# Kernel optimization log

Measured on AMD Instinct MI355X. Metric: run time of the kernel, lower is better.

## Reference

```python
import jax, jax.numpy as jnp
import numpy as np

EMBED_DIM = 768
NUM_HEADS = 12
HEAD_DIM = EMBED_DIM // NUM_HEADS


def setup_inputs() -> dict:
    key = jax.random.key(0)
    ks = jax.random.split(key, 6)
    B, N = 8, 1024
    x = jax.random.normal(ks[0], (B, N, EMBED_DIM), dtype=jnp.float32)
    pos_embedding = jax.random.normal(ks[1], (1, NUM_HEADS, N, N), dtype=jnp.float32)
    s_in = 1.0 / np.sqrt(EMBED_DIM)
    W_qkv = jax.random.normal(ks[2], (EMBED_DIM, 3 * EMBED_DIM), dtype=jnp.float32) * s_in
    b_qkv = jnp.zeros((3 * EMBED_DIM,), dtype=jnp.float32)
    W_proj = jax.random.normal(ks[3], (EMBED_DIM, EMBED_DIM), dtype=jnp.float32) * s_in
    b_proj = jnp.zeros((EMBED_DIM,), dtype=jnp.float32)
    return {"x": x, "pos_embedding": pos_embedding, "W_qkv": W_qkv,
            "b_qkv": b_qkv, "W_proj": W_proj, "b_proj": b_proj}


def reference(x, pos_embedding, W_qkv, b_qkv, W_proj, b_proj):
    B, N, C = x.shape
    H, D = NUM_HEADS, HEAD_DIM
    qkv = x @ W_qkv + b_qkv                      # [B,N,3C]
    qkv = qkv.reshape(B, N, 3, H, D)
    q = qkv[:, :, 0].transpose(0, 2, 1, 3)       # [B,H,N,D]
    k = qkv[:, :, 1].transpose(0, 2, 1, 3)
    v = qkv[:, :, 2].transpose(0, 2, 1, 3)
    # NOTE: bias is added BEFORE scaling, matching the original module.
    scores = (jnp.einsum('bhnd,bhmd->bhnm', q, k) + pos_embedding) / jnp.sqrt(
        jnp.asarray(D, dtype=x.dtype))
    attn = jax.nn.softmax(scores, axis=-1)       # dropout is identity in eval
    out = jnp.einsum('bhnm,bhmd->bhnd', attn, v)
    out = out.transpose(0, 2, 1, 3).reshape(B, N, C)
    return out @ W_proj + b_proj
```

## Files before the change

kernel.cpp:

```cpp
#include <hip/hip_runtime.h>

#define SEQ   1024
#define HEADS 12
#define CDIM  768
#define BATCH 8

#define QSCALE 0.18033688011112042f

typedef __attribute__((ext_vector_type(8))) short bf16x8;
typedef __attribute__((ext_vector_type(4))) float f32x4;
typedef __attribute__((ext_vector_type(16))) float f32x16;
typedef __attribute__((ext_vector_type(4))) float float4v;
typedef __attribute__((ext_vector_type(4))) short short4v;

__device__ __forceinline__ void gload_lds16(const void* g, void* l) {
  __builtin_amdgcn_global_load_lds(
      (const __attribute__((address_space(1))) unsigned int*)g,
      (__attribute__((address_space(3))) unsigned int*)l, 16, 0, 0);
}

__device__ __forceinline__ unsigned short f2bf(float f) {
  union { float f; unsigned u; } v; v.f = f;
  unsigned r = v.u + 0x7fff + ((v.u >> 16) & 1);
  return (unsigned short)(r >> 16);
}

__device__ __forceinline__ unsigned cvtpk(float a, float b) {
  unsigned r;
  asm("v_cvt_pk_bf16_f32 %0, %1, %2" : "=v"(r) : "v"(a), "v"(b));
  return r;
}

__device__ __forceinline__ float bfsel(unsigned u, int odd) {
  union { unsigned u; float f; } v;
  v.u = odd ? (u & 0xffff0000u) : (u << 16);
  return v.f;
}

__global__ __launch_bounds__(256) void prep_x_kernel(const float* __restrict__ x,
                                                     short* __restrict__ A) {
  int i = blockIdx.x * 256 + threadIdx.x;
  int r = i / 192;
  int c4 = (i % 192) * 4;
  float4v xv = *(const float4v*)(x + (size_t)r * 768 + c4);
  short4v hi;
#pragma unroll
  for (int j = 0; j < 4; ++j) hi[j] = (short)f2bf(xv[j]);
  *(short4v*)(A + (size_t)r * 768 + c4) = hi;
}

__global__ __launch_bounds__(256) void prep_w_kernel(const float* __restrict__ W,
                                                     short* __restrict__ Bt) {
  __shared__ float tile[64][65];
  int k0 = blockIdx.x * 64;
  int n0 = blockIdx.y * 64;
  int t = threadIdx.x;
#pragma unroll
  for (int it = 0; it < 16; ++it) {
    int r = it * 4 + (t >> 6);
    int c = t & 63;
    tile[r][c] = W[(size_t)(k0 + r) * 2304 + n0 + c];
  }
  __syncthreads();
#pragma unroll
  for (int it = 0; it < 16; ++it) {
    int nr = it * 4 + (t >> 6);
    int kc = t & 63;
    Bt[(size_t)(n0 + nr) * 768 + k0 + kc] = (short)f2bf(tile[kc][nr]);
  }
}

__global__ __launch_bounds__(256) void prep_wp_kernel(const float* __restrict__ W,
                                                      short* __restrict__ Bt) {
  __shared__ float tile[64][65];
  int k0 = blockIdx.x * 64;
  int n0 = blockIdx.y * 64;
  int t = threadIdx.x;
#pragma unroll
  for (int it = 0; it < 16; ++it) {
    int r = it * 4 + (t >> 6);
    int c = t & 63;
    tile[r][c] = W[(size_t)(k0 + r) * 768 + n0 + c];
  }
  __syncthreads();
#pragma unroll
  for (int it = 0; it < 16; ++it) {
    int nr = it * 4 + (t >> 6);
    int kc = t & 63;
    Bt[(size_t)(n0 + nr) * 768 + k0 + kc] = (short)f2bf(tile[kc][nr]);
  }
}

__global__ __launch_bounds__(256) void prep_pos_kernel(const float* __restrict__ P,
                                                       short* __restrict__ PB) {
  int t = blockIdx.x * 256 + threadIdx.x;
  int lane = t & 63;
  int jh   = (t >> 6) & 1;
  int i0   = (t >> 7) & 1;
  int w    = (t >> 8) & 3;
  int ti   = (t >> 10) & 15;
  int qblk = (t >> 14) & 7;
  int h    = t >> 17;
  int c5 = lane & 31, g1 = lane >> 5;
  int q = qblk * 128 + w * 32 + c5;
  const float* src = P + ((size_t)h * SEQ + q) * SEQ
                     + ti * 64 + i0 * 32 + 4 * g1 + 16 * jh;
  float4v v0 = *(const float4v*)(src);
  float4v v1 = *(const float4v*)(src + 8);
  union { short s[8]; bf16x8 v; } o;
#pragma unroll
  for (int p = 0; p < 4; ++p) {
    o.s[p]     = (short)f2bf(v0[p] * QSCALE);
    o.s[4 + p] = (short)f2bf(v1[p] * QSCALE);
  }
  *(bf16x8*)(PB + (size_t)t * 8) = o.v;
}

template <int MODE>
__global__ __launch_bounds__(512, 4) void gemm_kernel(
    const short* __restrict__ A, const short* __restrict__ Bt,
    const float* __restrict__ bias,
    short* __restrict__ outQ, short* __restrict__ outK, short* __restrict__ outVT,
    float* __restrict__ outF) {
  constexpr int NBLK = (MODE == 1) ? 18 : 6;
  constexpr int CHUNK = (MODE == 1) ? 144 : 48;
  const int bid = blockIdx.x;
  const int lb = (bid & 7) * CHUNK + (bid >> 3);
  const int n0 = (lb % NBLK) * 128;
  const int m0 = (lb / NBLK) * 128;

  __shared__ short Als[2][128 * 64];
  __shared__ short Bls[2][128 * 64];
  const int tid = threadIdx.x;
  const int lane = tid & 63;
  const int w = tid >> 6;
  const int wr = (w & 1) * 64;
  const int wc = (w >> 1) * 32;
  f32x4 acc[4][2];
#pragma unroll
  for (int mi = 0; mi < 4; ++mi)
#pragma unroll
    for (int ni = 0; ni < 2; ++ni) acc[mi][ni] = (f32x4){0.f, 0.f, 0.f, 0.f};

  auto STAGE = [&](int buf, int k0) {
#pragma unroll
    for (int pass = 0; pass < 2; ++pass) {
      int rbase = pass * 64 + w * 8;
      int row = rbase + (lane >> 3);
      int ul = (lane & 7) ^ (row & 7);
      gload_lds16(A + (size_t)(m0 + row) * 768 + k0 + ul * 8, Als[buf] + rbase * 64);
      gload_lds16(Bt + (size_t)(n0 + row) * 768 + k0 + ul * 8, Bls[buf] + rbase * 64);
    }
  };

  STAGE(0, 0);
  asm volatile("s_waitcnt vmcnt(0)" ::: "memory");
  __builtin_amdgcn_sched_barrier(0);
  __builtin_amdgcn_s_barrier();

  for (int t = 0; t < 12; ++t) {
    if (t < 11) STAGE((t + 1) & 1, (t + 1) * 64);
    const short* Ab = Als[t & 1];
    const short* Bb = Bls[t & 1];
    __builtin_amdgcn_s_setprio(1);
#pragma unroll
    for (int kk = 0; kk < 2; ++kk) {
      bf16x8 af[4], bfv[2];
#pragma unroll
      for (int mi = 0; mi < 4; ++mi) {
        int row = wr + mi * 16 + (lane & 15);
        int off = (row * 128 + kk * 64 + (lane >> 4) * 16) ^ ((row & 7) << 4);
        af[mi] = *(const bf16x8*)((const char*)Ab + off);
      }
#pragma unroll
      for (int ni = 0; ni < 2; ++ni) {
        int row = wc + ni * 16 + (lane & 15);
        int off = (row * 128 + kk * 64 + (lane >> 4) * 16) ^ ((row & 7) << 4);
        bfv[ni] = *(const bf16x8*)((const char*)Bb + off);
      }
#pragma unroll
      for (int mi = 0; mi < 4; ++mi)
#pragma unroll
        for (int ni = 0; ni < 2; ++ni)
          acc[mi][ni] = __builtin_amdgcn_mfma_f32_16x16x32_bf16(
              af[mi], bfv[ni], acc[mi][ni], 0, 0, 0);
    }
    __builtin_amdgcn_s_setprio(0);
    if (t < 11) {
      asm volatile("s_waitcnt vmcnt(0)" ::: "memory");
      __builtin_amdgcn_sched_barrier(0);
      __builtin_amdgcn_s_barrier();
    }
  }

  if (MODE == 1) {
    const int three = n0 / 768;
    const int nb = n0 - three * 768;
#pragma unroll
    for (int mi = 0; mi < 4; ++mi)
#pragma unroll
      for (int ni = 0; ni < 2; ++ni)
#pragma unroll
        for (int j = 0; j < 4; ++j) {
          int row = m0 + wr + mi * 16 + ((lane >> 4) << 2) + j;
          int col = n0 + wc + ni * 16 + (lane & 15);
          float v = acc[mi][ni][j] + bias[col];
          int rem = nb + wc + ni * 16 + (lane & 15);
          int hh = rem >> 6, d = rem & 63;
          int b = row >> 10, n = row & 1023;
          size_t bh = (size_t)(b * 12 + hh);
          if (three == 0)      outQ[(bh * 1024 + n) * 64 + d] = (short)f2bf(v * QSCALE);
          else if (three == 1) outK[(bh * 1024 + n) * 64 + d] = (short)f2bf(v);
          else                 outVT[(bh * 64 + d) * 1024 + n] = (short)f2bf(v);
        }
  } else {
#pragma unroll
    for (int mi = 0; mi < 4; ++mi)
#pragma unroll
      for (int ni = 0; ni < 2; ++ni)
#pragma unroll
        for (int j = 0; j < 4; ++j) {
          int row = m0 + wr + mi * 16 + ((lane >> 4) << 2) + j;
          int col = n0 + wc + ni * 16 + (lane & 15);
          outF[(size_t)row * 768 + col] = acc[mi][ni][j] + bias[col];
        }
  }
}

#define MKFRAG(B, pA, pB, pC, pD)                                    \
  { unsigned x0 = (pA), y0 = (pC), x1 = (pB), y1 = (pD);             \
    asm("v_permlane32_swap_b32 %0, %1" : "+v"(x0), "+v"(y0));        \
    asm("v_permlane32_swap_b32 %0, %1" : "+v"(x1), "+v"(y1));        \
    B.u[0] = x0; B.u[1] = x1; B.u[2] = y0; B.u[3] = y1; }

__global__ __launch_bounds__(256, 3) void attn_kernel(
    const short* __restrict__ qb, const short* __restrict__ kb,
    const short* __restrict__ vtb, const short* __restrict__ posb,
    short* __restrict__ outb) {
  const int bid = blockIdx.x;
  const int lb = (bid & 7) * 96 + (bid >> 3);
  const int qblk = lb & 7;
  const int hb = lb >> 3;
  const int h = hb >> 3, b = hb & 7;

  const int tid = threadIdx.x, lane = tid & 63, w = tid >> 6;
  const int c5 = lane & 31, g1 = lane >> 5;
  const size_t bh = (size_t)(b * 12 + h);
  const short* Q = qb + bh * SEQ * 64;
  const short* K = kb + bh * SEQ * 64;
  const short* VT = vtb + bh * 64 * SEQ;
  const int q0w = qblk * 128 + w * 32;

  const short* pwb = posb + (size_t)h * 1048576 + (size_t)qblk * 131072
                     + w * 2048 + lane * 8;

  __shared__ short kls[3 * 4096];
  __shared__ short vls[3 * 4096];

  bf16x8 qf[4];
#pragma unroll
  for (int kd = 0; kd < 4; ++kd)
    qf[kd] = *(const bf16x8*)(Q + (size_t)(q0w + c5) * 64 + kd * 16 + g1 * 8);

  f32x16 o0, o1;
#pragma unroll
  for (int i = 0; i < 16; ++i) { o0[i] = 0.f; o1[i] = 0.f; }
  float lsum = 0.f;

  auto STAGE = [&](short* kb_, short* vb_, int kv0) {
    int r0 = w * 8 + (lane >> 3);
    int u0 = (lane & 7) ^ (r0 & 7);
    gload_lds16(K + (size_t)(kv0 + r0) * 64 + u0 * 8, kb_ + w * 512);
    gload_lds16(K + (size_t)(kv0 + 32 + r0) * 64 + u0 * 8, kb_ + 2048 + w * 512);
    gload_lds16(VT + (size_t)r0 * SEQ + kv0 + u0 * 8, vb_ + w * 512);
    gload_lds16(VT + (size_t)(32 + r0) * SEQ + kv0 + u0 * 8, vb_ + 2048 + w * 512);
  };

  short* kbuf0 = kls;        short* vbuf0 = vls;
  short* kbuf1 = kls + 4096; short* vbuf1 = vls + 4096;
  short* kbuf2 = kls + 8192; short* vbuf2 = vls + 8192;

  union pb4 { bf16x8 v; unsigned u[4]; };
  pb4 ua0, ua1, ub0, ub1, na0, na1, nb0, nb1;
  ua0.v = *(const bf16x8*)(pwb);
  ua1.v = *(const bf16x8*)(pwb + 512);
  ub0.v = *(const bf16x8*)(pwb + 1024);
  ub1.v = *(const bf16x8*)(pwb + 1536);
  STAGE(kbuf0, vbuf0, 0);
  STAGE(kbuf1, vbuf1, 64);
  asm volatile("s_waitcnt vmcnt(4)" ::: "memory");
  __builtin_amdgcn_sched_barrier(0);
  __builtin_amdgcn_s_barrier();

  for (int ti = 0; ti < 16; ++ti) {
    const int kv0 = ti * 64;

    if (ti < 15) {
      const short* pnx = pwb + (ti + 1) * 8192;
      na0.v = *(const bf16x8*)(pnx);
      na1.v = *(const bf16x8*)(pnx + 512);
      nb0.v = *(const bf16x8*)(pnx + 1024);
      nb1.v = *(const bf16x8*)(pnx + 1536);
    }
    asm volatile("" ::: "memory");
    if (ti < 14) STAGE(kbuf2, vbuf2, kv0 + 128);

    const short* kc = kbuf0;
    const short* vc = vbuf0;

    f32x16 p0, p1;
#pragma unroll
    for (int i = 0; i < 16; ++i) { p0[i] = 0.f; p1[i] = 0.f; }
    __builtin_amdgcn_s_setprio(1);
#pragma unroll
    for (int kd = 0; kd < 4; ++kd) {
      int off0 = (c5 * 128 + kd * 32 + g1 * 16) ^ ((c5 & 7) << 4);
      int off1 = ((32 + c5) * 128 + kd * 32 + g1 * 16) ^ ((c5 & 7) << 4);
      bf16x8 kf0 = *(const bf16x8*)((const char*)kc + off0);
      bf16x8 kf1 = *(const bf16x8*)((const char*)kc + off1);
      p0 = __builtin_amdgcn_mfma_f32_32x32x16_bf16(kf0, qf[kd], p0, 0, 0, 0);
      p1 = __builtin_amdgcn_mfma_f32_32x32x16_bf16(kf1, qf[kd], p1, 0, 0, 0);
    }
    __builtin_amdgcn_s_setprio(0);

#pragma unroll
    for (int r = 0; r < 16; ++r) {
      unsigned wa = (r < 8) ? ua0.u[(r >> 1) & 3] : ua1.u[(r >> 1) & 3];
      unsigned wb = (r < 8) ? ub0.u[(r >> 1) & 3] : ub1.u[(r >> 1) & 3];
      float a = exp2f(p0[r] + bfsel(wa, r & 1));
      float bq = exp2f(p1[r] + bfsel(wb, r & 1));
      p0[r] = a; p1[r] = bq;
      lsum += a + bq;
    }

    unsigned pk0[8], pk1[8];
#pragma unroll
    for (int m = 0; m < 4; ++m) {
      pk0[2 * m]     = cvtpk(p0[4 * m],     p0[4 * m + 1]);
      pk0[2 * m + 1] = cvtpk(p0[4 * m + 2], p0[4 * m + 3]);
      pk1[2 * m]     = cvtpk(p1[4 * m],     p1[4 * m + 1]);
      pk1[2 * m + 1] = cvtpk(p1[4 * m + 2], p1[4 * m + 3]);
    }

    union bb { bf16x8 v; unsigned u[4]; } B0, B1, B2, B3;
    MKFRAG(B0, pk0[0], pk0[1], pk0[2], pk0[3]);
    MKFRAG(B1, pk0[4], pk0[5], pk0[6], pk0[7]);
    MKFRAG(B2, pk1[0], pk1[1], pk1[2], pk1[3]);
    MKFRAG(B3, pk1[4], pk1[5], pk1[6], pk1[7]);

    __builtin_amdgcn_s_setprio(1);
#define PVSTEP(Bv, s)                                                        \
    { int o0f = (c5 * 128 + (s) * 32 + g1 * 16) ^ ((c5 & 7) << 4);           \
      int o1f = ((32 + c5) * 128 + (s) * 32 + g1 * 16) ^ ((c5 & 7) << 4);    \
      bf16x8 vf0 = *(const bf16x8*)((const char*)vc + o0f);                  \
      bf16x8 vf1 = *(const bf16x8*)((const char*)vc + o1f);                  \
      o0 = __builtin_amdgcn_mfma_f32_32x32x16_bf16(vf0, Bv.v, o0, 0, 0, 0);  \
      o1 = __builtin_amdgcn_mfma_f32_32x32x16_bf16(vf1, Bv.v, o1, 0, 0, 0); }
    PVSTEP(B0, 0); PVSTEP(B1, 1); PVSTEP(B2, 2); PVSTEP(B3, 3);
#undef PVSTEP
    __builtin_amdgcn_s_setprio(0);

    if (ti < 15) { ua0 = na0; ua1 = na1; ub0 = nb0; ub1 = nb1; }
    short* tk = kbuf0; kbuf0 = kbuf1; kbuf1 = kbuf2; kbuf2 = tk;
    short* tv = vbuf0; vbuf0 = vbuf1; vbuf1 = vbuf2; vbuf2 = tv;

    if (ti < 15) {
      if (ti < 14) asm volatile("s_waitcnt vmcnt(4)" ::: "memory");
      else         asm volatile("s_waitcnt vmcnt(0)" ::: "memory");
      __builtin_amdgcn_sched_barrier(0);
      __builtin_amdgcn_s_barrier();
    }
  }

  lsum += __shfl_xor(lsum, 32);
  float inv = 1.0f / lsum;
  size_t obase = (size_t)(b * SEQ + q0w + c5) * 768 + h * 64 + g1 * 4;
#pragma unroll
  for (int m = 0; m < 4; ++m) {
    short4v ov0, ov1;
#pragma unroll
    for (int j = 0; j < 4; ++j) {
      ov0[j] = (short)f2bf(o0[4 * m + j] * inv);
      ov1[j] = (short)f2bf(o1[4 * m + j] * inv);
    }
    *(short4v*)(outb + obase + m * 8) = ov0;
    *(short4v*)(outb + obase + 32 + m * 8) = ov1;
  }
}

extern "C" void kernel_launch(void* const* d_in, const int* in_sizes, int n_in,
                              void* d_out, int out_size, void* d_ws, size_t ws_size,
                              hipStream_t stream) {
  const float* x      = (const float*)d_in[0];
  const float* pos    = (const float*)d_in[1];
  const float* W_qkv  = (const float*)d_in[2];
  const float* b_qkv  = (const float*)d_in[3];
  const float* W_proj = (const float*)d_in[4];
  const float* b_proj = (const float*)d_in[5];
  float* out = (float*)d_out;

  char* ws = (char*)d_ws;
  short* A       = (short*)(ws);
  short* attnbuf = (short*)(ws);
  short* Bt      = (short*)(ws + 12582912);
  short* wpt     = (short*)(ws + 16121856);
  short* qbuf    = (short*)(ws + 17301504);
  short* kbuf    = (short*)(ws + 29884416);
  short* vtbuf   = (short*)(ws + 42467328);
  short* posb    = (short*)(ws + 55050240);

  prep_x_kernel<<<6144, 256, 0, stream>>>(x, A);
  prep_w_kernel<<<dim3(12, 36), 256, 0, stream>>>(W_qkv, Bt);
  prep_wp_kernel<<<dim3(12, 12), 256, 0, stream>>>(W_proj, wpt);
  prep_pos_kernel<<<6144, 256, 0, stream>>>(pos, posb);
  gemm_kernel<1><<<1152, 512, 0, stream>>>(A, Bt, b_qkv,
                                           qbuf, kbuf, vtbuf, nullptr);
  attn_kernel<<<768, 256, 0, stream>>>(qbuf, kbuf, vtbuf, posb, attnbuf);
  gemm_kernel<2><<<384, 512, 0, stream>>>(attnbuf, wpt, b_proj,
                                          nullptr, nullptr, nullptr, out);
}
```

Measured before the change: 152.6 us.

## Merge prep kernels and overlap pos-bias conversion with QKV GEMM main loop

Folds the x, W_qkv and W_proj conversion kernels into one launch, which removes two kernel launches. The pos_embedding fp32-to-bf16 conversion moves out of its own kernel and into the QKV GEMM. Each GEMM thread loads and stores up to three 8-element chunks interleaved with the K-loop iterations, so this memory traffic can overlap with MFMA work. The cost is extra registers and global traffic inside the GEMM, which could lower occupancy or disturb its load pipeline.

Result: no change. 151.0 us (-1.0%).

```diff
diff --git a/kernel.cpp b/kernel.cpp
--- a/kernel.cpp
+++ b/kernel.cpp
@@ -37,83 +37,57 @@
   return v.f;
 }
 
-__global__ __launch_bounds__(256) void prep_x_kernel(const float* __restrict__ x,
-                                                     short* __restrict__ A) {
-  int i = blockIdx.x * 256 + threadIdx.x;
-  int r = i / 192;
-  int c4 = (i % 192) * 4;
-  float4v xv = *(const float4v*)(x + (size_t)r * 768 + c4);
-  short4v hi;
-#pragma unroll
-  for (int j = 0; j < 4; ++j) hi[j] = (short)f2bf(xv[j]);
-  *(short4v*)(A + (size_t)r * 768 + c4) = hi;
-}
-
-__global__ __launch_bounds__(256) void prep_w_kernel(const float* __restrict__ W,
-                                                     short* __restrict__ Bt) {
+__global__ __launch_bounds__(256) void prep_all_kernel(
+    const float* __restrict__ x, short* __restrict__ A,
+    const float* __restrict__ Wqkv, short* __restrict__ Bt,
+    const float* __restrict__ Wproj, short* __restrict__ wpt) {
   __shared__ float tile[64][65];
-  int k0 = blockIdx.x * 64;
-  int n0 = blockIdx.y * 64;
-  int t = threadIdx.x;
-#pragma unroll
-  for (int it = 0; it < 16; ++it) {
-    int r = it * 4 + (t >> 6);
-    int c = t & 63;
-    tile[r][c] = W[(size_t)(k0 + r) * 2304 + n0 + c];
+  const int bid = blockIdx.x;
+  const int t = threadIdx.x;
+  if (bid < 6144) {
+    int i = bid * 256 + t;
+    int r = i / 192;
+    int c4 = (i % 192) * 4;
+    float4v xv = *(const float4v*)(x + (size_t)r * 768 + c4);
+    short4v hi;
+#pragma unroll
+    for (int j = 0; j < 4; ++j) hi[j] = (short)f2bf(xv[j]);
+    *(short4v*)(A + (size_t)r * 768 + c4) = hi;
+  } else if (bid < 6576) {
+    int idx = bid - 6144;
+    int k0 = (idx % 12) * 64;
+    int n0 = (idx / 12) * 64;
+#pragma unroll
+    for (int it = 0; it < 16; ++it) {
+      int r = it * 4 + (t >> 6);
+      int c = t & 63;
+      tile[r][c] = Wqkv[(size_t)(k0 + r) * 2304 + n0 + c];
+    }
+    __syncthreads();
+#pragma unroll
+    for (int it = 0; it < 16; ++it) {
+      int nr = it * 4 + (t >> 6);
+      int kc = t & 63;
+      Bt[(size_t)(n0 + nr) * 768 + k0 + kc] = (short)f2bf(tile[kc][nr]);
+    }
+  } else {
+    int idx = bid - 6576;
+    int k0 = (idx % 12) * 64;
+    int n0 = (idx / 12) * 64;
+#pragma unroll
+    for (int it = 0; it < 16; ++it) {
+      int r = it * 4 + (t >> 6);
+      int c = t & 63;
+      tile[r][c] = Wproj[(size_t)(k0 + r) * 768 + n0 + c];
+    }
+    __syncthreads();
+#pragma unroll
+    for (int it = 0; it < 16; ++it) {
+      int nr = it * 4 + (t >> 6);
+      int kc = t & 63;
+      wpt[(size_t)(n0 + nr) * 768 + k0 + kc] = (short)f2bf(tile[kc][nr]);
+    }
   }
-  __syncthreads();
-#pragma unroll
-  for (int it = 0; it < 16; ++it) {
-    int nr = it * 4 + (t >> 6);
-    int kc = t & 63;
-    Bt[(size_t)(n0 + nr) * 768 + k0 + kc] = (short)f2bf(tile[kc][nr]);
-  }
-}
-
-__global__ __launch_bounds__(256) void prep_wp_kernel(const float* __restrict__ W,
-                                                      short* __restrict__ Bt) {
-  __shared__ float tile[64][65];
-  int k0 = blockIdx.x * 64;
-  int n0 = blockIdx.y * 64;
-  int t = threadIdx.x;
-#pragma unroll
-  for (int it = 0; it < 16; ++it) {
-    int r = it * 4 + (t >> 6);
-    int c = t & 63;
-    tile[r][c] = W[(size_t)(k0 + r) * 768 + n0 + c];
-  }
-  __syncthreads();
-#pragma unroll
-  for (int it = 0; it < 16; ++it) {
-    int nr = it * 4 + (t >> 6);
-    int kc = t & 63;
-    Bt[(size_t)(n0 + nr) * 768 + k0 + kc] = (short)f2bf(tile[kc][nr]);
-  }
-}
-
-__global__ __launch_bounds__(256) void prep_pos_kernel(const float* __restrict__ P,
-                                                       short* __restrict__ PB) {
-  int t = blockIdx.x * 256 + threadIdx.x;
-  int lane = t & 63;
-  int jh   = (t >> 6) & 1;
-  int i0   = (t >> 7) & 1;
-  int w    = (t >> 8) & 3;
-  int ti   = (t >> 10) & 15;
-  int qblk = (t >> 14) & 7;
-  int h    = t >> 17;
-  int c5 = lane & 31, g1 = lane >> 5;
-  int q = qblk * 128 + w * 32 + c5;
-  const float* src = P + ((size_t)h * SEQ + q) * SEQ
-                     + ti * 64 + i0 * 32 + 4 * g1 + 16 * jh;
-  float4v v0 = *(const float4v*)(src);
-  float4v v1 = *(const float4v*)(src + 8);
-  union { short s[8]; bf16x8 v; } o;
-#pragma unroll
-  for (int p = 0; p < 4; ++p) {
-    o.s[p]     = (short)f2bf(v0[p] * QSCALE);
-    o.s[4 + p] = (short)f2bf(v1[p] * QSCALE);
-  }
-  *(bf16x8*)(PB + (size_t)t * 8) = o.v;
 }
 
 template <int MODE>
@@ -121,7 +95,8 @@
     const short* __restrict__ A, const short* __restrict__ Bt,
     const float* __restrict__ bias,
     short* __restrict__ outQ, short* __restrict__ outK, short* __restrict__ outVT,
-    float* __restrict__ outF) {
+    float* __restrict__ outF,
+    const float* __restrict__ pos, short* __restrict__ posb) {
   constexpr int NBLK = (MODE == 1) ? 18 : 6;
   constexpr int CHUNK = (MODE == 1) ? 144 : 48;
   const int bid = blockIdx.x;
@@ -142,6 +117,27 @@
 #pragma unroll
     for (int ni = 0; ni < 2; ++ni) acc[mi][ni] = (f32x4){0.f, 0.f, 0.f, 0.f};
 
+  const int gtid = bid * 512 + tid;
+  const bool job3 = (bid < 768);
+  const float* pp = nullptr;
+  f32x4 pja, pjb;
+  auto pos_addr = [&](int j) -> const float* {
+    int ln = j & 63, jh = (j >> 6) & 1, i0 = (j >> 7) & 1, w4 = (j >> 8) & 3,
+        ti = (j >> 10) & 15, qb = (j >> 14) & 7, hh = j >> 17;
+    int q = qb * 128 + w4 * 32 + (ln & 31);
+    return pos + ((size_t)hh * SEQ + q) * SEQ + ti * 64 + i0 * 32
+           + 4 * (ln >> 5) + 16 * jh;
+  };
+  auto pos_store = [&](int j) {
+    union { short s[8]; bf16x8 v; } o;
+#pragma unroll
+    for (int p = 0; p < 4; ++p) {
+      o.s[p]     = (short)f2bf(pja[p] * QSCALE);
+      o.s[4 + p] = (short)f2bf(pjb[p] * QSCALE);
+    }
+    *(bf16x8*)(posb + (size_t)j * 8) = o.v;
+  };
+
   auto STAGE = [&](int buf, int k0) {
 #pragma unroll
     for (int pass = 0; pass < 2; ++pass) {
@@ -159,6 +155,24 @@
   __builtin_amdgcn_s_barrier();
 
   for (int t = 0; t < 12; ++t) {
+    if (MODE == 1) {
+      if (t == 0) {
+        pp = pos_addr(gtid);
+        pja = *(const float4v*)pp; pjb = *(const float4v*)(pp + 8);
+      } else if (t == 2) {
+        pos_store(gtid);
+      } else if (t == 3) {
+        pp = pos_addr(gtid + 589824);
+        pja = *(const float4v*)pp; pjb = *(const float4v*)(pp + 8);
+      } else if (t == 5) {
+        pos_store(gtid + 589824);
+      } else if (t == 6 && job3) {
+        pp = pos_addr(gtid + 1179648);
+        pja = *(const float4v*)pp; pjb = *(const float4v*)(pp + 8);
+      } else if (t == 8 && job3) {
+        pos_store(gtid + 1179648);
+      }
+    }
     if (t < 11) STAGE((t + 1) & 1, (t + 1) * 64);
     const short* Ab = Als[t & 1];
     const short* Bb = Bls[t & 1];
@@ -409,13 +423,12 @@
   short* vtbuf   = (short*)(ws + 42467328);
   short* posb    = (short*)(ws + 55050240);
 
-  prep_x_kernel<<<6144, 256, 0, stream>>>(x, A);
-  prep_w_kernel<<<dim3(12, 36), 256, 0, stream>>>(W_qkv, Bt);
-  prep_wp_kernel<<<dim3(12, 12), 256, 0, stream>>>(W_proj, wpt);
-  prep_pos_kernel<<<6144, 256, 0, stream>>>(pos, posb);
+  prep_all_kernel<<<6720, 256, 0, stream>>>(x, A, W_qkv, Bt, W_proj, wpt);
   gemm_kernel<1><<<1152, 512, 0, stream>>>(A, Bt, b_qkv,
-                                           qbuf, kbuf, vtbuf, nullptr);
+                                           qbuf, kbuf, vtbuf, nullptr,
+                                           pos, posb);
   attn_kernel<<<768, 256, 0, stream>>>(qbuf, kbuf, vtbuf, posb, attnbuf);
   gemm_kernel<2><<<384, 512, 0, stream>>>(attnbuf, wpt, b_proj,
-                                          nullptr, nullptr, nullptr, out);
-}
+                                          nullptr, nullptr, nullptr, out,
+                                          nullptr, nullptr);
+}
```
